# Kernel optimization log

Measured on AMD Instinct MI355X. Metric: run time of the kernel, lower is better.

The kernel has to match this reference:

```python
import jax, jax.numpy as jnp
import numpy as np

TS = 0.01  # Euler step size (module's `ts`)

N_X, N_U, N_FEAT = 32, 16, 512
BATCH, SEQ_LEN = 512, 2048


def setup_inputs() -> dict:
    key = jax.random.key(0)
    k0, k1, k2, k3 = jax.random.split(key, 4)
    x0_batch = jax.random.normal(k0, (BATCH, 1, N_X), dtype=jnp.float32)
    u_batch = jax.random.normal(k1, (BATCH, SEQ_LEN, N_U), dtype=jnp.float32)
    # 2-layer MLP state-space model: Linear(n_x+n_u, n_feat) -> Tanh -> Linear(n_feat, n_x)
    fan1 = N_X + N_U
    W1 = jax.random.normal(k2, (fan1, N_FEAT), dtype=jnp.float32) / np.sqrt(fan1).astype(np.float32)
    b1 = jnp.zeros((N_FEAT,), dtype=jnp.float32)
    W2 = jax.random.normal(k3, (N_FEAT, N_X), dtype=jnp.float32) / np.sqrt(N_FEAT).astype(np.float32)
    b2 = jnp.zeros((N_X,), dtype=jnp.float32)
    return {"x0_batch": x0_batch, "u_batch": u_batch, "W1": W1, "b1": b1, "W2": W2, "b2": b2}


def reference(x0_batch, u_batch, W1, b1, W2, b2):
    # x0_batch: (B, 1, n_x); u_batch: (B, T, n_u) -> out: (B, T, n_x)
    x0 = x0_batch[:, 0, :]                       # (B, n_x)
    u_t = jnp.swapaxes(u_batch, 0, 1)            # (T, B, n_u) for scan over time

    def step(x, u):
        h = jnp.tanh(jnp.concatenate([x, u], axis=-1) @ W1 + b1)  # (B, n_feat)
        dx = h @ W2 + b2                                           # (B, n_x)
        x_next = x + TS * dx
        return x_next, x_next

    _, xs = jax.lax.scan(step, x0, u_t)          # xs: (T, B, n_x)
    return jnp.swapaxes(xs, 0, 1)                # (B, T, n_x)
```

## Files before the change

kernel.cpp:

```cpp
#include <hip/hip_runtime.h>

constexpr int NX = 32, NU = 16, NF = 512;
constexpr int SEQ = 2048;
constexpr int NT = 256;

__device__ __forceinline__ float fast_tanh(float y) {
    y = fminf(15.f, fmaxf(-15.f, y));
    float e = __expf(2.f * y);
    return (e - 1.f) * __builtin_amdgcn_rcpf(e + 1.f);
}

template<int CTRL>
__device__ __forceinline__ float dpp_add(float v) {
    int t = __builtin_amdgcn_update_dpp(0, __float_as_int(v), CTRL, 0xF, 0xF, true);
    return v + __int_as_float(t);
}

__global__ __launch_bounds__(NT, 2)
void fes_kernel(const float* __restrict__ x0, const float* __restrict__ ug,
                const float* __restrict__ W1, const float* __restrict__ b1,
                const float* __restrict__ W2, const float* __restrict__ b2,
                float* __restrict__ out)
{
    __shared__ float4 xs4[NX / 4];
    __shared__ float4 hs4[NF / 4];

    const int tid = threadIdx.x;
    const int row = blockIdx.x;
    const int f1  = tid + NT;
    const int sl  = tid >> 4;
    const int l   = tid & 15;
    const int j0  = sl, j1 = sl + 16;

    float w1a[48], w1b[48];
#pragma unroll
    for (int k = 0; k < 48; ++k) {
        w1a[k] = W1[k * NF + tid];
        w1b[k] = W1[k * NF + f1];
    }
    const float b1a = b1[tid], b1b = b1[f1];

    float w2a[32], w2b[32];
#pragma unroll
    for (int i = 0; i < 8; ++i)
#pragma unroll
        for (int c = 0; c < 4; ++c) {
            const int f = 4 * (l + 16 * i) + c;
            w2a[4 * i + c] = 0.01f * W2[f * NX + j0];
            w2b[4 * i + c] = 0.01f * W2[f * NX + j1];
        }
    const float bb0 = 0.01f * b2[j0], bb1 = 0.01f * b2[j1];

    float xr0 = x0[row * NX + j0];
    float xr1 = x0[row * NX + j1];

    const float4* ug4    = (const float4*)(ug + (size_t)row * SEQ * NU);
    float*        out_row = out + (size_t)row * SEQ * NX;

    if (tid < NX / 4) xs4[tid] = ((const float4*)(x0 + row * NX))[tid];

    float4 u0 = ug4[0], u1 = ug4[1], u2 = ug4[2], u3 = ug4[3];
    __syncthreads();

    for (int t = 0; t < SEQ; ++t) {
        float p0 = b1a, p1 = 0.f, p2 = 0.f, p3 = 0.f;
        float q0 = b1b, q1 = 0.f, q2 = 0.f, q3 = 0.f;
#pragma unroll
        for (int kk = 0; kk < 8; ++kk) {
            const float4 xv = xs4[kk];
            p0 = fmaf(w1a[4*kk],   xv.x, p0);
            p1 = fmaf(w1a[4*kk+1], xv.y, p1);
            p2 = fmaf(w1a[4*kk+2], xv.z, p2);
            p3 = fmaf(w1a[4*kk+3], xv.w, p3);
            q0 = fmaf(w1b[4*kk],   xv.x, q0);
            q1 = fmaf(w1b[4*kk+1], xv.y, q1);
            q2 = fmaf(w1b[4*kk+2], xv.z, q2);
            q3 = fmaf(w1b[4*kk+3], xv.w, q3);
        }
        p0 = fmaf(w1a[32], u0.x, p0); p1 = fmaf(w1a[33], u0.y, p1);
        p2 = fmaf(w1a[34], u0.z, p2); p3 = fmaf(w1a[35], u0.w, p3);
        p0 = fmaf(w1a[36], u1.x, p0); p1 = fmaf(w1a[37], u1.y, p1);
        p2 = fmaf(w1a[38], u1.z, p2); p3 = fmaf(w1a[39], u1.w, p3);
        p0 = fmaf(w1a[40], u2.x, p0); p1 = fmaf(w1a[41], u2.y, p1);
        p2 = fmaf(w1a[42], u2.z, p2); p3 = fmaf(w1a[43], u2.w, p3);
        p0 = fmaf(w1a[44], u3.x, p0); p1 = fmaf(w1a[45], u3.y, p1);
        p2 = fmaf(w1a[46], u3.z, p2); p3 = fmaf(w1a[47], u3.w, p3);
        q0 = fmaf(w1b[32], u0.x, q0); q1 = fmaf(w1b[33], u0.y, q1);
        q2 = fmaf(w1b[34], u0.z, q2); q3 = fmaf(w1b[35], u0.w, q3);
        q0 = fmaf(w1b[36], u1.x, q0); q1 = fmaf(w1b[37], u1.y, q1);
        q2 = fmaf(w1b[38], u1.z, q2); q3 = fmaf(w1b[39], u1.w, q3);
        q0 = fmaf(w1b[40], u2.x, q0); q1 = fmaf(w1b[41], u2.y, q1);
        q2 = fmaf(w1b[42], u2.z, q2); q3 = fmaf(w1b[43], u2.w, q3);
        q0 = fmaf(w1b[44], u3.x, q0); q1 = fmaf(w1b[45], u3.y, q1);
        q2 = fmaf(w1b[46], u3.z, q2); q3 = fmaf(w1b[47], u3.w, q3);

        const float h0 = fast_tanh((p0 + p1) + (p2 + p3));
        const float h1 = fast_tanh((q0 + q1) + (q2 + q3));
        ((float*)hs4)[tid] = h0;
        ((float*)hs4)[f1]  = h1;

        const int tn = (t + 1 < SEQ) ? t + 1 : t;
        const float4 n0 = ug4[4 * tn];
        const float4 n1 = ug4[4 * tn + 1];
        const float4 n2 = ug4[4 * tn + 2];
        const float4 n3 = ug4[4 * tn + 3];
        __syncthreads();

        float sa0 = 0.f, sa1 = 0.f, sa2 = 0.f, sa3 = 0.f;
        float sb0 = 0.f, sb1 = 0.f, sb2 = 0.f, sb3 = 0.f;
        const float* hsp = (const float*)hs4;
#pragma unroll
        for (int i = 0; i < 8; ++i) {
            const float4 hv = *(const float4*)&hsp[4 * (l + 16 * i)];
            sa0 = fmaf(hv.x, w2a[4*i],   sa0);
            sa1 = fmaf(hv.y, w2a[4*i+1], sa1);
            sa2 = fmaf(hv.z, w2a[4*i+2], sa2);
            sa3 = fmaf(hv.w, w2a[4*i+3], sa3);
            sb0 = fmaf(hv.x, w2b[4*i],   sb0);
            sb1 = fmaf(hv.y, w2b[4*i+1], sb1);
            sb2 = fmaf(hv.z, w2b[4*i+2], sb2);
            sb3 = fmaf(hv.w, w2b[4*i+3], sb3);
        }
        float sa = (sa0 + sa1) + (sa2 + sa3);
        float sb = (sb0 + sb1) + (sb2 + sb3);
        sa = dpp_add<0xB1>(sa);   sb = dpp_add<0xB1>(sb);
        sa = dpp_add<0x4E>(sa);   sb = dpp_add<0x4E>(sb);
        sa = dpp_add<0x124>(sa);  sb = dpp_add<0x124>(sb);
        sa = dpp_add<0x128>(sa);  sb = dpp_add<0x128>(sb);

        const float xn0 = xr0 + (sa + bb0);
        const float xn1 = xr1 + (sb + bb1);
        xr0 = xn0; xr1 = xn1;
        if (l == 0) {
            ((float*)xs4)[j0] = xn0;
            ((float*)xs4)[j1] = xn1;
            out_row[(size_t)t * NX + j0] = xn0;
            out_row[(size_t)t * NX + j1] = xn1;
        }
        u0 = n0; u1 = n1; u2 = n2; u3 = n3;
        __syncthreads();
    }
}

extern "C" void kernel_launch(void* const* d_in, const int* in_sizes, int n_in,
                              void* d_out, int out_size, void* d_ws, size_t ws_size,
                              hipStream_t stream) {
    const float* x0 = (const float*)d_in[0];
    const float* ug = (const float*)d_in[1];
    const float* W1 = (const float*)d_in[2];
    const float* b1 = (const float*)d_in[3];
    const float* W2 = (const float*)d_in[4];
    const float* b2 = (const float*)d_in[5];
    float* out = (float*)d_out;

    fes_kernel<<<dim3(512), dim3(NT), 0, stream>>>(x0, ug, W1, b1, W2, b2, out);
}
```

Measured before the change: 1.792 ms.

## Split layer-1 K across lane pairs, stage input chunks in LDS, cheaper tanh

Layer 1 is repartitioned so each thread pair covers 4 features with the 48-wide K split in half. The halves are combined with a single DPP add, and each thread then writes two tanh outputs. Inputs u are staged into shared memory in 32-step chunks instead of being prefetched per step from global memory. Tanh is rewritten as 1 - 2/(exp2(scaled y)+1), with the scale folded into W1 and b1, which drops the clamp and multiply. The chunk load adds a barrier every 32 steps and a per-step branchy select, and removing the clamp relies on the exp2/rcp hardware behaving at extremes.

```diff
diff --git a/kernel.cpp b/kernel.cpp
--- a/kernel.cpp
+++ b/kernel.cpp
@@ -2,18 +2,20 @@
 
 constexpr int NX = 32, NU = 16, NF = 512;
 constexpr int SEQ = 2048;
+constexpr int CH = 32;
 constexpr int NT = 256;
-
-__device__ __forceinline__ float fast_tanh(float y) {
-    y = fminf(15.f, fmaxf(-15.f, y));
-    float e = __expf(2.f * y);
-    return (e - 1.f) * __builtin_amdgcn_rcpf(e + 1.f);
-}
+constexpr float SC = 2.88539008177792681f;
 
 template<int CTRL>
 __device__ __forceinline__ float dpp_add(float v) {
     int t = __builtin_amdgcn_update_dpp(0, __float_as_int(v), CTRL, 0xF, 0xF, true);
     return v + __int_as_float(t);
+}
+
+__device__ __forceinline__ float tanh4(float y) {
+    const float e = __builtin_amdgcn_exp2f(y);
+    const float r = __builtin_amdgcn_rcpf(e + 1.f);
+    return fmaf(-2.f, r, 1.f);
 }
 
 __global__ __launch_bounds__(NT, 2)
@@ -24,21 +26,22 @@
 {
     __shared__ float4 xs4[NX / 4];
     __shared__ float4 hs4[NF / 4];
+    __shared__ float4 us4[CH * NU / 4];
 
-    const int tid = threadIdx.x;
-    const int row = blockIdx.x;
-    const int f1  = tid + NT;
-    const int sl  = tid >> 4;
-    const int l   = tid & 15;
+    const int tid = threadIdx.x, row = blockIdx.x;
+    const int g   = tid >> 1, kh = tid & 1;
+    const int sl  = tid >> 4, l  = tid & 15;
     const int j0  = sl, j1 = sl + 16;
 
-    float w1a[48], w1b[48];
+    float w1r[96];
 #pragma unroll
-    for (int k = 0; k < 48; ++k) {
-        w1a[k] = W1[k * NF + tid];
-        w1b[k] = W1[k * NF + f1];
-    }
-    const float b1a = b1[tid], b1b = b1[f1];
+    for (int i = 0; i < 24; ++i)
+#pragma unroll
+        for (int c = 0; c < 4; ++c)
+            w1r[i * 4 + c] = SC * W1[(kh * 24 + i) * NF + 4 * g + c];
+    float b1s[4];
+#pragma unroll
+    for (int c = 0; c < 4; ++c) b1s[c] = kh ? 0.f : SC * b1[4 * g + c];
 
     float w2a[32], w2b[32];
 #pragma unroll
@@ -54,91 +57,87 @@
     float xr0 = x0[row * NX + j0];
     float xr1 = x0[row * NX + j1];
 
-    const float4* ug4    = (const float4*)(ug + (size_t)row * SEQ * NU);
-    float*        out_row = out + (size_t)row * SEQ * NX;
+    const float* ug_row  = ug  + (size_t)row * SEQ * NU;
+    float*       out_row = out + (size_t)row * SEQ * NX;
 
     if (tid < NX / 4) xs4[tid] = ((const float4*)(x0 + row * NX))[tid];
 
-    float4 u0 = ug4[0], u1 = ug4[1], u2 = ug4[2], u3 = ug4[3];
-    __syncthreads();
+    const float4* bA = kh ? xs4 + 6 : xs4;
 
-    for (int t = 0; t < SEQ; ++t) {
-        float p0 = b1a, p1 = 0.f, p2 = 0.f, p3 = 0.f;
-        float q0 = b1b, q1 = 0.f, q2 = 0.f, q3 = 0.f;
-#pragma unroll
-        for (int kk = 0; kk < 8; ++kk) {
-            const float4 xv = xs4[kk];
-            p0 = fmaf(w1a[4*kk],   xv.x, p0);
-            p1 = fmaf(w1a[4*kk+1], xv.y, p1);
-            p2 = fmaf(w1a[4*kk+2], xv.z, p2);
-            p3 = fmaf(w1a[4*kk+3], xv.w, p3);
-            q0 = fmaf(w1b[4*kk],   xv.x, q0);
-            q1 = fmaf(w1b[4*kk+1], xv.y, q1);
-            q2 = fmaf(w1b[4*kk+2], xv.z, q2);
-            q3 = fmaf(w1b[4*kk+3], xv.w, q3);
-        }
-        p0 = fmaf(w1a[32], u0.x, p0); p1 = fmaf(w1a[33], u0.y, p1);
-        p2 = fmaf(w1a[34], u0.z, p2); p3 = fmaf(w1a[35], u0.w, p3);
-        p0 = fmaf(w1a[36], u1.x, p0); p1 = fmaf(w1a[37], u1.y, p1);
-        p2 = fmaf(w1a[38], u1.z, p2); p3 = fmaf(w1a[39], u1.w, p3);
-        p0 = fmaf(w1a[40], u2.x, p0); p1 = fmaf(w1a[41], u2.y, p1);
-        p2 = fmaf(w1a[42], u2.z, p2); p3 = fmaf(w1a[43], u2.w, p3);
-        p0 = fmaf(w1a[44], u3.x, p0); p1 = fmaf(w1a[45], u3.y, p1);
-        p2 = fmaf(w1a[46], u3.z, p2); p3 = fmaf(w1a[47], u3.w, p3);
-        q0 = fmaf(w1b[32], u0.x, q0); q1 = fmaf(w1b[33], u0.y, q1);
-        q2 = fmaf(w1b[34], u0.z, q2); q3 = fmaf(w1b[35], u0.w, q3);
-        q0 = fmaf(w1b[36], u1.x, q0); q1 = fmaf(w1b[37], u1.y, q1);
-        q2 = fmaf(w1b[38], u1.z, q2); q3 = fmaf(w1b[39], u1.w, q3);
-        q0 = fmaf(w1b[40], u2.x, q0); q1 = fmaf(w1b[41], u2.y, q1);
-        q2 = fmaf(w1b[42], u2.z, q2); q3 = fmaf(w1b[43], u2.w, q3);
-        q0 = fmaf(w1b[44], u3.x, q0); q1 = fmaf(w1b[45], u3.y, q1);
-        q2 = fmaf(w1b[46], u3.z, q2); q3 = fmaf(w1b[47], u3.w, q3);
-
-        const float h0 = fast_tanh((p0 + p1) + (p2 + p3));
-        const float h1 = fast_tanh((q0 + q1) + (q2 + q3));
-        ((float*)hs4)[tid] = h0;
-        ((float*)hs4)[f1]  = h1;
-
-        const int tn = (t + 1 < SEQ) ? t + 1 : t;
-        const float4 n0 = ug4[4 * tn];
-        const float4 n1 = ug4[4 * tn + 1];
-        const float4 n2 = ug4[4 * tn + 2];
-        const float4 n3 = ug4[4 * tn + 3];
+    for (int t0 = 0; t0 < SEQ; t0 += CH) {
+        if (tid < CH * NU / 4)
+            us4[tid] = *(const float4*)&ug_row[(size_t)t0 * NU + tid * 4];
         __syncthreads();
 
-        float sa0 = 0.f, sa1 = 0.f, sa2 = 0.f, sa3 = 0.f;
-        float sb0 = 0.f, sb1 = 0.f, sb2 = 0.f, sb3 = 0.f;
-        const float* hsp = (const float*)hs4;
+#pragma unroll 1
+        for (int tc = 0; tc < CH; ++tc) {
+            const int t = t0 + tc;
+            const float4* bB = kh ? us4 + tc * 4 - 2 : xs4;
+            const float4 iv0 = bA[0], iv1 = bA[1];
+            const float4 iv2 = bB[2], iv3 = bB[3], iv4 = bB[4], iv5 = bB[5];
+            float a0 = b1s[0], a1 = b1s[1], a2 = b1s[2], a3 = b1s[3];
+#define G1F4(iv, q)                                                        \
+            a0 = fmaf(w1r[(q)*16 + 0],  iv.x, a0);                         \
+            a1 = fmaf(w1r[(q)*16 + 1],  iv.x, a1);                         \
+            a2 = fmaf(w1r[(q)*16 + 2],  iv.x, a2);                         \
+            a3 = fmaf(w1r[(q)*16 + 3],  iv.x, a3);                         \
+            a0 = fmaf(w1r[(q)*16 + 4],  iv.y, a0);                         \
+            a1 = fmaf(w1r[(q)*16 + 5],  iv.y, a1);                         \
+            a2 = fmaf(w1r[(q)*16 + 6],  iv.y, a2);                         \
+            a3 = fmaf(w1r[(q)*16 + 7],  iv.y, a3);                         \
+            a0 = fmaf(w1r[(q)*16 + 8],  iv.z, a0);                         \
+            a1 = fmaf(w1r[(q)*16 + 9],  iv.z, a1);                         \
+            a2 = fmaf(w1r[(q)*16 + 10], iv.z, a2);                         \
+            a3 = fmaf(w1r[(q)*16 + 11], iv.z, a3);                         \
+            a0 = fmaf(w1r[(q)*16 + 12], iv.w, a0);                         \
+            a1 = fmaf(w1r[(q)*16 + 13], iv.w, a1);                         \
+            a2 = fmaf(w1r[(q)*16 + 14], iv.w, a2);                         \
+            a3 = fmaf(w1r[(q)*16 + 15], iv.w, a3);
+            G1F4(iv0, 0) G1F4(iv1, 1) G1F4(iv2, 2)
+            G1F4(iv3, 3) G1F4(iv4, 4) G1F4(iv5, 5)
+#undef G1F4
+            a0 = dpp_add<0xB1>(a0);
+            a1 = dpp_add<0xB1>(a1);
+            a2 = dpp_add<0xB1>(a2);
+            a3 = dpp_add<0xB1>(a3);
+            float2 hw;
+            hw.x = tanh4(kh ? a2 : a0);
+            hw.y = tanh4(kh ? a3 : a1);
+            ((float2*)hs4)[g * 2 + kh] = hw;
+            __syncthreads();
+
+            float sa0 = 0.f, sa1 = 0.f, sa2 = 0.f, sa3 = 0.f;
+            float sb0 = 0.f, sb1 = 0.f, sb2 = 0.f, sb3 = 0.f;
 #pragma unroll
-        for (int i = 0; i < 8; ++i) {
-            const float4 hv = *(const float4*)&hsp[4 * (l + 16 * i)];
-            sa0 = fmaf(hv.x, w2a[4*i],   sa0);
-            sa1 = fmaf(hv.y, w2a[4*i+1], sa1);
-            sa2 = fmaf(hv.z, w2a[4*i+2], sa2);
-            sa3 = fmaf(hv.w, w2a[4*i+3], sa3);
-            sb0 = fmaf(hv.x, w2b[4*i],   sb0);
-            sb1 = fmaf(hv.y, w2b[4*i+1], sb1);
-            sb2 = fmaf(hv.z, w2b[4*i+2], sb2);
-            sb3 = fmaf(hv.w, w2b[4*i+3], sb3);
+            for (int i = 0; i < 8; ++i) {
+                const float4 hv = hs4[l + 16 * i];
+                sa0 = fmaf(hv.x, w2a[4*i],   sa0);
+                sa1 = fmaf(hv.y, w2a[4*i+1], sa1);
+                sa2 = fmaf(hv.z, w2a[4*i+2], sa2);
+                sa3 = fmaf(hv.w, w2a[4*i+3], sa3);
+                sb0 = fmaf(hv.x, w2b[4*i],   sb0);
+                sb1 = fmaf(hv.y, w2b[4*i+1], sb1);
+                sb2 = fmaf(hv.z, w2b[4*i+2], sb2);
+                sb3 = fmaf(hv.w, w2b[4*i+3], sb3);
+            }
+            float sa = (sa0 + sa1) + (sa2 + sa3);
+            float sb = (sb0 + sb1) + (sb2 + sb3);
+            sa = dpp_add<0xB1>(sa);   sb = dpp_add<0xB1>(sb);
+            sa = dpp_add<0x4E>(sa);   sb = dpp_add<0x4E>(sb);
+            sa = dpp_add<0x124>(sa);  sb = dpp_add<0x124>(sb);
+            sa = dpp_add<0x128>(sa);  sb = dpp_add<0x128>(sb);
+
+            const float xn0 = xr0 + (sa + bb0);
+            const float xn1 = xr1 + (sb + bb1);
+            xr0 = xn0; xr1 = xn1;
+            if (l < 2) {
+                const float v  = l ? xn1 : xn0;
+                const int   jj = j0 + (l << 4);
+                ((float*)xs4)[jj] = v;
+                out_row[(size_t)t * NX + jj] = v;
+            }
+            __syncthreads();
         }
-        float sa = (sa0 + sa1) + (sa2 + sa3);
-        float sb = (sb0 + sb1) + (sb2 + sb3);
-        sa = dpp_add<0xB1>(sa);   sb = dpp_add<0xB1>(sb);
-        sa = dpp_add<0x4E>(sa);   sb = dpp_add<0x4E>(sb);
-        sa = dpp_add<0x124>(sa);  sb = dpp_add<0x124>(sb);
-        sa = dpp_add<0x128>(sa);  sb = dpp_add<0x128>(sb);
-
-        const float xn0 = xr0 + (sa + bb0);
-        const float xn1 = xr1 + (sb + bb1);
-        xr0 = xn0; xr1 = xn1;
-        if (l == 0) {
-            ((float*)xs4)[j0] = xn0;
-            ((float*)xs4)[j1] = xn1;
-            out_row[(size_t)t * NX + j0] = xn0;
-            out_row[(size_t)t * NX + j1] = xn1;
-        }
-        u0 = n0; u1 = n1; u2 = n2; u3 = n3;
-        __syncthreads();
     }
 }
 
```

Result: faster. 1.747 ms (-2.5%).
